# Optimization experiments

Hardware: AMD Instinct MI355X
Metric: run time of the kernel (lower is better)

## Reference

```python
import jax, jax.numpy as jnp
import numpy as np

HIDDEN = 1024
HEADS = 8
HEAD_DIM = HIDDEN // HEADS  # 128
MAX_SEQ = 4096
MAX_TOKS = 2048
THETA = 10000.0
INIT_STD = 0.02


def setup_inputs() -> dict:
    key = jax.random.key(0)
    ks = jax.random.split(key, 8)
    B, L = 2, 4096
    hidden_states = jax.random.normal(ks[0], (B, L, HIDDEN), dtype=jnp.float32)
    attention_mask = jnp.ones((B, L), dtype=bool)
    segment_ids = jnp.sort(jax.random.randint(ks[1], (B, L), 0, 2), axis=-1).astype(jnp.int32)
    position_ids = jnp.sort(jax.random.randint(ks[2], (B, L), 0, MAX_SEQ), axis=-1).astype(jnp.int32)
    # nn.Linear weights stored (out_features, in_features), bias=False, normal(0, 0.02)
    wq = (jax.random.normal(ks[3], (HIDDEN, HIDDEN), dtype=jnp.float32) * INIT_STD)
    wk = (jax.random.normal(ks[4], (HIDDEN, HIDDEN), dtype=jnp.float32) * INIT_STD)
    wv = (jax.random.normal(ks[5], (HIDDEN, HIDDEN), dtype=jnp.float32) * INIT_STD)
    wo = (jax.random.normal(ks[6], (HIDDEN, HIDDEN), dtype=jnp.float32) * INIT_STD)
    return {
        "hidden_states": hidden_states,
        "wq": wq, "wk": wk, "wv": wv, "wo": wo,
        "attention_mask": attention_mask,
        "segment_ids": segment_ids,
        "position_ids": position_ids,
    }


def _freqs_cis(position_ids):
    # precompute_freqs_cis gathered at position_ids -> (B, L, HEAD_DIM//2) complex
    inv_freq = 1.0 / (THETA ** (jnp.arange(0, HEAD_DIM, 2, dtype=jnp.float32) / HEAD_DIM))
    ang = position_ids.astype(jnp.float32)[..., None] * inv_freq  # (B,L,D/2)
    return jax.lax.complex(jnp.cos(ang), jnp.sin(ang))


def _apply_rope(x, fc):
    # x: (B,L,H,D); fc: (B,L,D/2) complex; broadcast fc over heads
    xs = x.astype(jnp.float32).reshape(*x.shape[:-1], HEAD_DIM // 2, 2)
    xc = jax.lax.complex(xs[..., 0], xs[..., 1])  # (B,L,H,D/2)
    out = xc * fc[:, :, None, :]
    return jnp.stack([jnp.real(out), jnp.imag(out)], axis=-1).reshape(x.shape).astype(x.dtype)


def reference(hidden_states, wq, wk, wv, wo, attention_mask, segment_ids, position_ids):
    B, L, _ = hidden_states.shape
    q = (hidden_states @ wq.T).reshape(B, L, HEADS, HEAD_DIM)
    k = (hidden_states @ wk.T).reshape(B, L, HEADS, HEAD_DIM)
    v = (hidden_states @ wv.T).reshape(B, L, HEADS, HEAD_DIM)

    fc = _freqs_cis(position_ids)
    q = _apply_rope(q, fc)
    k = _apply_rope(k, fc)

    # block-causal mask: query block index >= key block index
    blk = jnp.arange(L) // MAX_TOKS
    causal = blk[:, None] >= blk[None, :]                                   # (L,L)
    seg = (segment_ids[:, :, None] == segment_ids[:, None, :])              # (B,L,L)
    mask = attention_mask[:, None, None, :] & seg[:, None, :, :] & causal[None, None, :, :]

    scale = 1.0 / np.float32(np.sqrt(HEAD_DIM))
    scores = jnp.einsum('bqhd,bkhd->bhqk', q, k) * scale                    # (B,H,L,L)
    scores = jnp.where(mask, scores, jnp.float32(-jnp.inf))
    probs = jax.nn.softmax(scores, axis=-1)
    attn = jnp.einsum('bhqk,bkhd->bqhd', probs, v).reshape(B, L, HIDDEN)
    return attn @ wo.T
```

## Files before the change

kernel.cpp:

```cpp
#include <hip/hip_runtime.h>
#include <hip/hip_bf16.h>
#include <cstdint>
#include <cstddef>
#include <type_traits>

#define HID 1024
#define HEADS 8
#define HDIM 128
#define SEQ 4096
#define BATCH 2

typedef float f32x4 __attribute__((ext_vector_type(4)));
typedef float f32x16 __attribute__((ext_vector_type(16)));
typedef short bf16x8 __attribute__((ext_vector_type(8)));
typedef unsigned short u16x8 __attribute__((ext_vector_type(8)));

typedef bf16x8 __attribute__((may_alias)) bf16x8_a;
typedef u16x8  __attribute__((may_alias)) u16x8_a;
typedef float4 __attribute__((may_alias)) float4_a;
typedef unsigned int __attribute__((may_alias)) u32_a;

__device__ __forceinline__ unsigned short f2bf(float f) {
    union { float f; unsigned int u; } v; v.f = f;
    unsigned int u = v.u;
    unsigned int r = (u + 0x7FFFu + ((u >> 16) & 1u)) >> 16;
    return (unsigned short)r;
}
__device__ __forceinline__ float bf2f(unsigned short h) {
    union { unsigned int u; float f; } v; v.u = ((unsigned int)h) << 16;
    return v.f;
}

__device__ __forceinline__ void plane_swap(unsigned int& x, unsigned int& y) {
    asm("v_permlane32_swap_b32 %0, %1" : "+v"(x), "+v"(y));
}
__device__ __forceinline__ unsigned int cvt_pk(float lo, float hi) {
    unsigned int r;
    asm("v_cvt_pk_bf16_f32 %0, %1, %2" : "=v"(r) : "v"(lo), "v"(hi));
    return r;
}
__device__ __forceinline__ bf16x8 pack4(unsigned int a, unsigned int b,
                                        unsigned int c, unsigned int d) {
    union { unsigned int u[4]; bf16x8 v; } t;
    t.u[0] = a; t.u[1] = b; t.u[2] = c; t.u[3] = d;
    return t.v;
}

__global__ __launch_bounds__(256)
void cvt_kernel(const float* __restrict__ X, unsigned short* __restrict__ Y)
{
    int i = (blockIdx.x * 256 + threadIdx.x) * 8;
    float4 d0 = *(const float4_a*)&X[i];
    float4 d1 = *(const float4_a*)&X[i + 4];
    u16x8 t;
    t[0] = f2bf(d0.x); t[1] = f2bf(d0.y); t[2] = f2bf(d0.z); t[3] = f2bf(d0.w);
    t[4] = f2bf(d1.x); t[5] = f2bf(d1.y); t[6] = f2bf(d1.z); t[7] = f2bf(d1.w);
    *(u16x8_a*)&Y[i] = t;
}

__global__ __launch_bounds__(256)
void cvtw_kernel(const float* __restrict__ w0, const float* __restrict__ w1,
                 const float* __restrict__ w2, const float* __restrict__ w3,
                 unsigned short* __restrict__ Y)
{
    const int WSZ8 = (HID * HID) / 8;
    int c = blockIdx.x * 256 + threadIdx.x;
    int quarter = c >> 17;
    int idx = (c & (WSZ8 - 1)) * 8;
    const float* w = quarter == 0 ? w0 : quarter == 1 ? w1 : quarter == 2 ? w2 : w3;
    float4 d0 = *(const float4_a*)&w[idx];
    float4 d1 = *(const float4_a*)&w[idx + 4];
    u16x8 t;
    t[0] = f2bf(d0.x); t[1] = f2bf(d0.y); t[2] = f2bf(d0.z); t[3] = f2bf(d0.w);
    t[4] = f2bf(d1.x); t[5] = f2bf(d1.y); t[6] = f2bf(d1.z); t[7] = f2bf(d1.w);
    *(u16x8_a*)&Y[(size_t)quarter * HID * HID + idx] = t;
}

template<bool A_BF16, bool B_BF16, typename OutT>
__global__ __launch_bounds__(256)
void gemm_bt(const void* __restrict__ Av, const void* __restrict__ Bv,
             OutT* __restrict__ C, int M, int N, int K, int lda)
{
    __shared__ __align__(16) unsigned short Al[128][72];
    __shared__ __align__(16) unsigned short Bl[128][72];
    const int tid  = threadIdx.x;
    const int lane = tid & 63;
    const int w    = tid >> 6;
    const int wr   = w >> 1, wc = w & 1;
    const int l16  = lane & 15, l4 = lane >> 4;
    const int tm   = blockIdx.y * 128, tn = blockIdx.x * 128;

    f32x4 acc[4][4] = {};

    for (int ko = 0; ko < K; ko += 64) {
        __syncthreads();
#pragma unroll
        for (int it = 0; it < 4; ++it) {
            int c = tid + 256 * it;
            int row = c >> 3, col0 = (c & 7) * 8;
            if constexpr (A_BF16) {
                const unsigned short* A = (const unsigned short*)Av;
                *(u16x8_a*)&Al[row][col0] =
                    *(const u16x8_a*)&A[(size_t)(tm + row) * lda + ko + col0];
            } else {
                const float* A = (const float*)Av;
                const float* p = &A[(size_t)(tm + row) * lda + ko + col0];
                float4 d0 = *(const float4_a*)p;
                float4 d1 = *(const float4_a*)(p + 4);
                u16x8 t;
                t[0] = f2bf(d0.x); t[1] = f2bf(d0.y); t[2] = f2bf(d0.z); t[3] = f2bf(d0.w);
                t[4] = f2bf(d1.x); t[5] = f2bf(d1.y); t[6] = f2bf(d1.z); t[7] = f2bf(d1.w);
                *(u16x8_a*)&Al[row][col0] = t;
            }
            if constexpr (B_BF16) {
                const unsigned short* B = (const unsigned short*)Bv;
                *(u16x8_a*)&Bl[row][col0] =
                    *(const u16x8_a*)&B[(size_t)(tn + row) * K + ko + col0];
            } else {
                const float* B = (const float*)Bv;
                const float* p = &B[(size_t)(tn + row) * K + ko + col0];
                float4 d0 = *(const float4_a*)p;
                float4 d1 = *(const float4_a*)(p + 4);
                u16x8 t;
                t[0] = f2bf(d0.x); t[1] = f2bf(d0.y); t[2] = f2bf(d0.z); t[3] = f2bf(d0.w);
                t[4] = f2bf(d1.x); t[5] = f2bf(d1.y); t[6] = f2bf(d1.z); t[7] = f2bf(d1.w);
                *(u16x8_a*)&Bl[row][col0] = t;
            }
        }
        __syncthreads();
#pragma unroll
        for (int kk = 0; kk < 2; ++kk) {
            bf16x8 af[4], bfr[4];
#pragma unroll
            for (int i = 0; i < 4; ++i)
                af[i] = *(const bf16x8_a*)&Al[wr*64 + i*16 + l16][kk*32 + l4*8];
#pragma unroll
            for (int j = 0; j < 4; ++j)
                bfr[j] = *(const bf16x8_a*)&Bl[wc*64 + j*16 + l16][kk*32 + l4*8];
#pragma unroll
            for (int i = 0; i < 4; ++i)
#pragma unroll
                for (int j = 0; j < 4; ++j)
                    acc[i][j] = __builtin_amdgcn_mfma_f32_16x16x32_bf16(af[i], bfr[j], acc[i][j], 0, 0, 0);
        }
    }
#pragma unroll
    for (int i = 0; i < 4; ++i)
#pragma unroll
        for (int j = 0; j < 4; ++j)
#pragma unroll
            for (int r = 0; r < 4; ++r) {
                int row = tm + wr*64 + i*16 + l4*4 + r;
                int col = tn + wc*64 + j*16 + l16;
                if constexpr (std::is_same<OutT, float>::value)
                    C[(size_t)row * N + col] = acc[i][j][r];
                else
                    C[(size_t)row * N + col] = f2bf(acc[i][j][r]);
            }
}

template<int HSH>
__global__ __launch_bounds__(256)
void rope_kernel(unsigned short* __restrict__ X, const int* __restrict__ pos_ids, int RS)
{
    int c = blockIdx.x * 256 + threadIdx.x;
    int d0 = (c & 15) * 8;
    int h  = (c >> 4) & ((1 << HSH) - 1);
    int l  = (c >> (4 + HSH)) & 4095;
    int b  = c >> (16 + HSH);
    int pos = pos_ids[b * SEQ + l];
    size_t off = (size_t)(b * SEQ + l) * RS + h * HDIM + d0;
    u16x8 d = *(const u16x8_a*)&X[off];
    float x[8];
#pragma unroll
    for (int j = 0; j < 8; ++j) x[j] = bf2f(d[j]);
#pragma unroll
    for (int j = 0; j < 4; ++j) {
        int i = (d0 >> 1) + j;
        float invf = powf(10000.0f, -(float)i * (1.0f / 64.0f));
        float ang = (float)pos * invf;
        float s, cth;
        sincosf(ang, &s, &cth);
        float o0 = x[2*j] * cth - x[2*j+1] * s;
        float o1 = x[2*j] * s   + x[2*j+1] * cth;
        d[2*j]   = f2bf(o0);
        d[2*j+1] = f2bf(o1);
    }
    *(u16x8_a*)&X[off] = d;
}

__global__ __launch_bounds__(256, 2)
void attn_kernel(const unsigned short* Q,
                 const unsigned short* K,
                 const unsigned short* V,
                 const int* __restrict__ seg,
                 unsigned short* O, int RS)
{
    __shared__ __align__(16) unsigned short Kl[64][136];
    __shared__ __align__(16) unsigned short Vt[128][72];

    const int tid  = threadIdx.x;
    const int lane = tid & 63;
    const int l32  = lane & 31, hi = lane >> 5;
    const int w    = tid >> 6;
    const int qt = (SEQ / 128 - 1) - blockIdx.x;
    const int h  = blockIdx.y;
    const int b  = blockIdx.z;
    const int qg0 = qt * 128 + w * 32;
    const int hoff = h * HDIM;

    bf16x8 qf[8];
    {
        size_t base = (size_t)(b * SEQ + qg0 + l32) * RS + hoff;
#pragma unroll
        for (int kk = 0; kk < 8; ++kk)
            qf[kk] = *(const bf16x8_a*)&Q[base + kk*16 + hi*8];
    }

    f32x16 acco0 = {}, acco1 = {}, acco2 = {}, acco3 = {};
    float lsum = 0.f;

    const int nkt = ((qt >> 4) + 1) * 32;

    int lo = 0, hb = SEQ;
    while (lo < hb) { int mid = (lo + hb) >> 1; if (seg[b * SEQ + mid] == 0) lo = mid + 1; else hb = mid; }
    const int boundary = lo;
    const bool blk_seg1 = (seg[b * SEQ + qt * 128] == 1);
    const bool blk_seg0 = (seg[b * SEQ + qt * 128 + 127] == 0);
    const bool mixed = !blk_seg0 && !blk_seg1;
    int kstart = 0, kend = nkt;
    if (blk_seg1) kstart = boundary >> 6;
    if (blk_seg0) {
        int ke = (boundary + 63) >> 6;
        kend = ke < nkt ? ke : nkt;
    }
    const bool qlt = (qg0 + l32) < boundary;

    const int kp = tid & 31, db = tid >> 5;
    const float sc = 0.08838834764831845f;

    u16x8 kreg[4], v0a, v0b, v1a, v1b;
    {
        const int kb = kstart * 64;
#pragma unroll
        for (int it = 0; it < 4; ++it) {
            int c = tid + 256 * it;
            kreg[it] = *(const u16x8_a*)&K[(size_t)(b * SEQ + kb + (c >> 4)) * RS + hoff + (c & 15) * 8];
        }
        size_t vb0 = (size_t)(b * SEQ + kb + 2 * kp) * RS + hoff + db * 16;
        size_t vb1 = (size_t)(b * SEQ + kb + 2 * kp + 1) * RS + hoff + db * 16;
        v0a = *(const u16x8_a*)&V[vb0];     v0b = *(const u16x8_a*)&V[vb0 + 8];
        v1a = *(const u16x8_a*)&V[vb1];     v1b = *(const u16x8_a*)&V[vb1 + 8];
    }

    for (int kt = kstart; kt < kend; ++kt) {
        const int kb = kt * 64;
        __syncthreads();
#pragma unroll
        for (int it = 0; it < 4; ++it) {
            int c = tid + 256 * it;
            *(u16x8_a*)&Kl[c >> 4][(c & 15) * 8] = kreg[it];
        }
#pragma unroll
        for (int j = 0; j < 8; ++j) {
            *(u32_a*)&Vt[db * 16 + j][2 * kp] =
                (unsigned int)(unsigned short)v0a[j] | ((unsigned int)(unsigned short)v1a[j] << 16);
            *(u32_a*)&Vt[db * 16 + 8 + j][2 * kp] =
                (unsigned int)(unsigned short)v0b[j] | ((unsigned int)(unsigned short)v1b[j] << 16);
        }
        __syncthreads();

        if (kt + 1 < kend) {
            const int kb2 = (kt + 1) * 64;
#pragma unroll
            for (int it = 0; it < 4; ++it) {
                int c = tid + 256 * it;
                kreg[it] = *(const u16x8_a*)&K[(size_t)(b * SEQ + kb2 + (c >> 4)) * RS + hoff + (c & 15) * 8];
            }
            size_t vb0 = (size_t)(b * SEQ + kb2 + 2 * kp) * RS + hoff + db * 16;
            size_t vb1 = (size_t)(b * SEQ + kb2 + 2 * kp + 1) * RS + hoff + db * 16;
            v0a = *(const u16x8_a*)&V[vb0];     v0b = *(const u16x8_a*)&V[vb0 + 8];
            v1a = *(const u16x8_a*)&V[vb1];     v1b = *(const u16x8_a*)&V[vb1 + 8];
        }

        f32x16 a0 = {}, a1 = {};
#pragma unroll
        for (int kk = 0; kk < 8; ++kk) {
            bf16x8 k0 = *(const bf16x8_a*)&Kl[     l32][kk*16 + hi*8];
            bf16x8 k1 = *(const bf16x8_a*)&Kl[32 + l32][kk*16 + hi*8];
            a0 = __builtin_amdgcn_mfma_f32_32x32x16_bf16(k0, qf[kk], a0, 0, 0, 0);
            a1 = __builtin_amdgcn_mfma_f32_32x32x16_bf16(k1, qf[kk], a1, 0, 0, 0);
        }

        unsigned int pk0[8], pk1[8];
        const bool need_mask = mixed || (kb < boundary && kb + 64 > boundary);
        if (need_mask) {
            const int kb0 = kb + 4 * hi, kb1 = kb + 32 + 4 * hi;
#pragma unroll
            for (int i = 0; i < 8; ++i) {
                int r0 = 2 * i;
                int off = (r0 & 3) + 8 * (r0 >> 2);
                float p0 = ((kb0 + off     < boundary) == qlt) ? __expf(a0[r0]     * sc) : 0.0f;
                float p1 = ((kb0 + off + 1 < boundary) == qlt) ? __expf(a0[r0 + 1] * sc) : 0.0f;
                float q0 = ((kb1 + off     < boundary) == qlt) ? __expf(a1[r0]     * sc) : 0.0f;
                float q1 = ((kb1 + off + 1 < boundary) == qlt) ? __expf(a1[r0 + 1] * sc) : 0.0f;
                lsum += (p0 + p1) + (q0 + q1);
                pk0[i] = cvt_pk(p0, p1);
                pk1[i] = cvt_pk(q0, q1);
            }
        } else {
#pragma unroll
            for (int i = 0; i < 8; ++i) {
                int r0 = 2 * i;
                float p0 = __expf(a0[r0]     * sc);
                float p1 = __expf(a0[r0 + 1] * sc);
                float q0 = __expf(a1[r0]     * sc);
                float q1 = __expf(a1[r0 + 1] * sc);
                lsum += (p0 + p1) + (q0 + q1);
                pk0[i] = cvt_pk(p0, p1);
                pk1[i] = cvt_pk(q0, q1);
            }
        }
        plane_swap(pk0[0], pk0[2]); plane_swap(pk0[1], pk0[3]);
        plane_swap(pk0[4], pk0[6]); plane_swap(pk0[5], pk0[7]);
        plane_swap(pk1[0], pk1[2]); plane_swap(pk1[1], pk1[3]);
        plane_swap(pk1[4], pk1[6]); plane_swap(pk1[5], pk1[7]);
        bf16x8 pf[4];
        pf[0] = pack4(pk0[0], pk0[1], pk0[2], pk0[3]);
        pf[1] = pack4(pk0[4], pk0[5], pk0[6], pk0[7]);
        pf[2] = pack4(pk1[0], pk1[1], pk1[2], pk1[3]);
        pf[3] = pack4(pk1[4], pk1[5], pk1[6], pk1[7]);

#pragma unroll
        for (int ks = 0; ks < 4; ++ks) {
            bf16x8 vf0 = *(const bf16x8_a*)&Vt[      l32][ks*16 + hi*8];
            bf16x8 vf1 = *(const bf16x8_a*)&Vt[32  + l32][ks*16 + hi*8];
            bf16x8 vf2 = *(const bf16x8_a*)&Vt[64  + l32][ks*16 + hi*8];
            bf16x8 vf3 = *(const bf16x8_a*)&Vt[96  + l32][ks*16 + hi*8];
            acco0 = __builtin_amdgcn_mfma_f32_32x32x16_bf16(pf[ks], vf0, acco0, 0, 0, 0);
            acco1 = __builtin_amdgcn_mfma_f32_32x32x16_bf16(pf[ks], vf1, acco1, 0, 0, 0);
            acco2 = __builtin_amdgcn_mfma_f32_32x32x16_bf16(pf[ks], vf2, acco2, 0, 0, 0);
            acco3 = __builtin_amdgcn_mfma_f32_32x32x16_bf16(pf[ks], vf3, acco3, 0, 0, 0);
        }
    }

    float tot = lsum + __shfl_xor(lsum, 32, 64);
#pragma unroll
    for (int r = 0; r < 16; ++r) {
        int qrow = (r & 3) + 8 * (r >> 2) + 4 * hi;
        float inv = 1.0f / __shfl(tot, qrow, 64);
        size_t base = (size_t)(b * SEQ + qg0 + qrow) * RS + hoff;
        O[base +       l32] = f2bf(acco0[r] * inv);
        O[base +  32 + l32] = f2bf(acco1[r] * inv);
        O[base +  64 + l32] = f2bf(acco2[r] * inv);
        O[base +  96 + l32] = f2bf(acco3[r] * inv);
    }
}

extern "C" void kernel_launch(void* const* d_in, const int* in_sizes, int n_in,
                              void* d_out, int out_size, void* d_ws, size_t ws_size,
                              hipStream_t stream)
{
    const float* X  = (const float*)d_in[0];
    const float* wq = (const float*)d_in[1];
    const float* wk = (const float*)d_in[2];
    const float* wv = (const float*)d_in[3];
    const float* wo = (const float*)d_in[4];
    const int* seg = (const int*)d_in[n_in - 2];
    const int* pos = (const int*)d_in[n_in - 1];
    float* out = (float*)d_out;

    const size_t NTOK = (size_t)BATCH * SEQ;
    const size_t MAT  = NTOK * HID;
    const size_t WSZ  = (size_t)HID * HID;

    if (ws_size >= (4 * MAT + 4 * WSZ) * sizeof(unsigned short)) {
        unsigned short* QKVb = (unsigned short*)d_ws;
        unsigned short* Xb   = QKVb + 3 * MAT;
        unsigned short* Wb   = Xb + MAT;
        unsigned short* Wob  = Wb + 3 * WSZ;

        cvt_kernel<<<(int)(MAT / (256 * 8)), 256, 0, stream>>>(X, Xb);
        cvtw_kernel<<<(int)(4 * WSZ / (256 * 8)), 256, 0, stream>>>(wq, wk, wv, wo, Wb);

        dim3 gq(3 * HID / 128, (int)(NTOK / 128));
        gemm_bt<true, true, unsigned short><<<gq, 256, 0, stream>>>(
            (const void*)Xb, (const void*)Wb, QKVb, (int)NTOK, 3 * HID, HID, HID);

        rope_kernel<4><<<(BATCH * SEQ * 16 * 16) / 256, 256, 0, stream>>>(QKVb, pos, 3 * HID);

        dim3 ga(SEQ / 128, HEADS, BATCH);
        attn_kernel<<<ga, 256, 0, stream>>>(QKVb, QKVb + HID, QKVb + 2 * HID, seg,
                                            QKVb , 3 * HID);

        dim3 go(HID / 128, (int)(NTOK / 128));
        gemm_bt<true, true, float><<<go, 256, 0, stream>>>(
            (const void*)QKVb, (const void*)Wob, out, (int)NTOK, HID, HID, 3 * HID);
    } else {
        unsigned short* Qb = (unsigned short*)d_ws;
        unsigned short* Kb = Qb + MAT;
        unsigned short* Vb = Kb + MAT;

        dim3 gg(HID / 128, (int)(NTOK / 128));
        gemm_bt<false, false, unsigned short><<<gg, 256, 0, stream>>>(
            (const void*)X, (const void*)wq, Qb, (int)NTOK, HID, HID, HID);
        gemm_bt<false, false, unsigned short><<<gg, 256, 0, stream>>>(
            (const void*)X, (const void*)wk, Kb, (int)NTOK, HID, HID, HID);
        gemm_bt<false, false, unsigned short><<<gg, 256, 0, stream>>>(
            (const void*)X, (const void*)wv, Vb, (int)NTOK, HID, HID, HID);

        rope_kernel<3><<<(BATCH * SEQ * HEADS * 16) / 256, 256, 0, stream>>>(Qb, pos, HID);
        rope_kernel<3><<<(BATCH * SEQ * HEADS * 16) / 256, 256, 0, stream>>>(Kb, pos, HID);

        dim3 ga(SEQ / 128, HEADS, BATCH);
        attn_kernel<<<ga, 256, 0, stream>>>(Qb, Kb, Vb, seg, Qb, HID);

        gemm_bt<true, false, float><<<gg, 256, 0, stream>>>(
            (const void*)Qb, (const void*)wo, out, (int)NTOK, HID, HID, HID);
    }
}
```

Measured before the change: 237.1 us.

## Use direct global-to-LDS loads with XOR-swizzled layout in bf16 GEMMs

Adds a new GEMM kernel that loads A and B tiles with global_load_lds, writing straight into shared memory without staging through registers. The tiles use an XOR-swizzled 64-wide layout in place of the padded 72-wide rows, to avoid bank conflicts when MFMA fragments are read. Both the QKV projection and the output projection now use it. The goal is less register pressure and fewer VALU and LDS-store instructions in the load path. The loop is still single-buffered with two barriers per k-step, so loads are not overlapped with compute.

```diff
diff --git a/kernel.cpp b/kernel.cpp
--- a/kernel.cpp
+++ b/kernel.cpp
@@ -44,6 +44,11 @@
     union { unsigned int u[4]; bf16x8 v; } t;
     t.u[0] = a; t.u[1] = b; t.u[2] = c; t.u[3] = d;
     return t.v;
+}
+__device__ __forceinline__ void g2lds16(const unsigned short* g, unsigned short* l) {
+    __builtin_amdgcn_global_load_lds(
+        (const __attribute__((address_space(1))) void*)g,
+        (__attribute__((address_space(3))) void*)l, 16, 0, 0);
 }
 
 __global__ __launch_bounds__(256)
@@ -74,6 +79,66 @@
     t[0] = f2bf(d0.x); t[1] = f2bf(d0.y); t[2] = f2bf(d0.z); t[3] = f2bf(d0.w);
     t[4] = f2bf(d1.x); t[5] = f2bf(d1.y); t[6] = f2bf(d1.z); t[7] = f2bf(d1.w);
     *(u16x8_a*)&Y[(size_t)quarter * HID * HID + idx] = t;
+}
+
+template<typename OutT>
+__global__ __launch_bounds__(256)
+void gemm_swz(const unsigned short* __restrict__ A, const unsigned short* __restrict__ B,
+              OutT* __restrict__ C, int M, int N, int K, int lda)
+{
+    __shared__ __align__(16) unsigned short Al[128][64];
+    __shared__ __align__(16) unsigned short Bl[128][64];
+    const int tid  = threadIdx.x;
+    const int lane = tid & 63;
+    const int w    = tid >> 6;
+    const int wr   = w >> 1, wc = w & 1;
+    const int l16  = lane & 15, l4 = lane >> 4;
+    const int tm   = blockIdx.y * 128, tn = blockIdx.x * 128;
+    const int srow  = lane >> 3;
+    const int sslot = (lane & 7) ^ srow;
+
+    f32x4 acc[4][4] = {};
+
+    for (int ko = 0; ko < K; ko += 64) {
+        __syncthreads();
+#pragma unroll
+        for (int it = 0; it < 4; ++it) {
+            int ca = w * 4 + it;
+            int row = ca * 8 + srow;
+            g2lds16(&A[(size_t)(tm + row) * lda + ko + sslot * 8], &Al[ca * 8][0]);
+            g2lds16(&B[(size_t)(tn + row) * K   + ko + sslot * 8], &Bl[ca * 8][0]);
+        }
+        __syncthreads();
+#pragma unroll
+        for (int kk = 0; kk < 2; ++kk) {
+            const int rslot = (kk * 4 + l4) ^ (l16 & 7);
+            bf16x8 af[4], bfr[4];
+#pragma unroll
+            for (int i = 0; i < 4; ++i)
+                af[i] = *(const bf16x8_a*)&Al[wr*64 + i*16 + l16][rslot * 8];
+#pragma unroll
+            for (int j = 0; j < 4; ++j)
+                bfr[j] = *(const bf16x8_a*)&Bl[wc*64 + j*16 + l16][rslot * 8];
+#pragma unroll
+            for (int i = 0; i < 4; ++i)
+#pragma unroll
+                for (int j = 0; j < 4; ++j)
+                    acc[i][j] = __builtin_amdgcn_mfma_f32_16x16x32_bf16(af[i], bfr[j], acc[i][j], 0, 0, 0);
+        }
+    }
+#pragma unroll
+    for (int i = 0; i < 4; ++i)
+#pragma unroll
+        for (int j = 0; j < 4; ++j)
+#pragma unroll
+            for (int r = 0; r < 4; ++r) {
+                int row = tm + wr*64 + i*16 + l4*4 + r;
+                int col = tn + wc*64 + j*16 + l16;
+                if constexpr (std::is_same<OutT, float>::value)
+                    C[(size_t)row * N + col] = acc[i][j][r];
+                else
+                    C[(size_t)row * N + col] = f2bf(acc[i][j][r]);
+            }
 }
 
 template<bool A_BF16, bool B_BF16, typename OutT>
@@ -384,8 +449,8 @@
         cvtw_kernel<<<(int)(4 * WSZ / (256 * 8)), 256, 0, stream>>>(wq, wk, wv, wo, Wb);
 
         dim3 gq(3 * HID / 128, (int)(NTOK / 128));
-        gemm_bt<true, true, unsigned short><<<gq, 256, 0, stream>>>(
-            (const void*)Xb, (const void*)Wb, QKVb, (int)NTOK, 3 * HID, HID, HID);
+        gemm_swz<unsigned short><<<gq, 256, 0, stream>>>(
+            Xb, Wb, QKVb, (int)NTOK, 3 * HID, HID, HID);
 
         rope_kernel<4><<<(BATCH * SEQ * 16 * 16) / 256, 256, 0, stream>>>(QKVb, pos, 3 * HID);
 
@@ -394,8 +459,8 @@
                                             QKVb , 3 * HID);
 
         dim3 go(HID / 128, (int)(NTOK / 128));
-        gemm_bt<true, true, float><<<go, 256, 0, stream>>>(
-            (const void*)QKVb, (const void*)Wob, out, (int)NTOK, HID, HID, 3 * HID);
+        gemm_swz<float><<<go, 256, 0, stream>>>(
+            QKVb, Wob, out, (int)NTOK, HID, HID, 3 * HID);
     } else {
         unsigned short* Qb = (unsigned short*)d_ws;
         unsigned short* Kb = Qb + MAT;
```

Result: faster. 229.2 us (-3.3%).
